# Kernel tuning notes

Hardware: AMD Instinct MI355X
Metric: run time of the kernel (lower is better)

The kernel has to match this reference:

```python
import jax, jax.numpy as jnp
import numpy as np

B, S, D_MODEL = 2, 2048, 2048
H, DS, DG, DV = 16, 64, 64, 128
ROPE_BASE = 10000.0
NEG_INF = -1e9


def _rope(x, base=ROPE_BASE):
    # x: [B, S, H, D] -> rotate-half RoPE over positions 0..S-1
    d = x.shape[-1]
    half = d // 2
    inv_freq = 1.0 / (base ** (jnp.arange(half, dtype=jnp.float32) / half))
    ang = jnp.arange(x.shape[1], dtype=jnp.float32)[:, None] * inv_freq  # [S, half]
    cos = jnp.cos(ang)[None, :, None, :]
    sin = jnp.sin(ang)[None, :, None, :]
    x1, x2 = x[..., :half], x[..., half:]
    return jnp.concatenate([x1 * cos - x2 * sin, x1 * sin + x2 * cos], axis=-1)


def setup_inputs() -> dict:
    key = jax.random.key(0)
    ks = jax.random.split(key, 8)
    s = lambda fan_in: 1.0 / np.sqrt(fan_in)
    return {
        "x": jax.random.normal(ks[0], (B, S, D_MODEL), dtype=jnp.float32),
        "wq_sem": jax.random.normal(ks[1], (D_MODEL, H * DS), dtype=jnp.float32) * s(D_MODEL),
        "wk_sem": jax.random.normal(ks[2], (D_MODEL, H * DS), dtype=jnp.float32) * s(D_MODEL),
        "wq_geo": jax.random.normal(ks[3], (D_MODEL, H * DG), dtype=jnp.float32) * s(D_MODEL),
        "wk_geo": jax.random.normal(ks[4], (D_MODEL, H * DG), dtype=jnp.float32) * s(D_MODEL),
        "wv": jax.random.normal(ks[5], (D_MODEL, H * DV), dtype=jnp.float32) * s(D_MODEL),
        "wo": jax.random.normal(ks[6], (H * DV, D_MODEL), dtype=jnp.float32) * s(H * DV),
        "gate_logit": jax.random.normal(ks[7], (H,), dtype=jnp.float32),
    }


def reference(x, wq_sem, wk_sem, wq_geo, wk_geo, wv, wo, gate_logit):
    b, sl, _ = x.shape
    # Projections -> [B, S, H, d]
    qs = (x @ wq_sem).reshape(b, sl, H, DS)
    ksem = (x @ wk_sem).reshape(b, sl, H, DS)
    qg = _rope((x @ wq_geo).reshape(b, sl, H, DG))
    kg = _rope((x @ wk_geo).reshape(b, sl, H, DG))
    v = (x @ wv).reshape(b, sl, H, DV)

    sem_scale = 1.0 / np.sqrt(DS)
    geo_scale = 1.0 / np.sqrt(DG)
    sem_scores = jnp.einsum("bqhd,bkhd->bhqk", qs, ksem) * sem_scale
    geo_scores = jnp.einsum("bqhd,bkhd->bhqk", qg, kg) * geo_scale

    # Learned per-head gate mixing semantic vs geometric paths
    g = jax.nn.sigmoid(gate_logit)[None, :, None, None]
    scores = g * sem_scores + (1.0 - g) * geo_scores

    causal = jnp.tril(jnp.ones((sl, sl), dtype=bool))
    scores = jnp.where(causal[None, None], scores, NEG_INF)
    attn = jax.nn.softmax(scores, axis=-1)

    out = jnp.einsum("bhqk,bkhd->bqhd", attn, v).reshape(b, sl, H * DV)
    return out @ wo
```

## Files before the change

kernel.cpp:

```cpp
#include <hip/hip_runtime.h>
#include <hip/hip_bf16.h>

typedef unsigned short u16;
typedef __attribute__((ext_vector_type(4))) float floatx4;
typedef __attribute__((ext_vector_type(8))) __bf16 bf16x8;

__device__ __forceinline__ u16 f2bf(float f) {
  unsigned int x = __builtin_bit_cast(unsigned int, f);
  unsigned int r = (x + 0x7fffu + ((x >> 16) & 1u)) >> 16;
  return (u16)r;
}
__device__ __forceinline__ float bf2f(u16 u) {
  unsigned int x = ((unsigned int)u) << 16;
  return __builtin_bit_cast(float, x);
}
__device__ __forceinline__ floatx4 mfma16(bf16x8 a, bf16x8 b, floatx4 c) {
  return __builtin_amdgcn_mfma_f32_16x16x32_bf16(a, b, c, 0, 0, 0);
}
__device__ __forceinline__ void gload16(const u16* g, u16* l) {
  __builtin_amdgcn_global_load_lds(
      (const __attribute__((address_space(1))) unsigned int*)g,
      (__attribute__((address_space(3))) unsigned int*)l, 16, 0, 0);
}
#define SCHEDB() __builtin_amdgcn_sched_barrier(0)
#define SBAR() __builtin_amdgcn_s_barrier()

#define BB 2
#define SS 2048
#define DM 2048
#define HH 16
#define PCOLS 6144

__global__ void prep_all_k(const float* __restrict__ x,
                           const float* w0, const float* w1, const float* w2,
                           const float* w3, const float* w4, const float* w5,
                           u16* __restrict__ WcatT, u16* __restrict__ WoT,
                           u16* __restrict__ Xbf,
                           float* __restrict__ cosT, float* __restrict__ sinT) {
  const int z = blockIdx.z;
  const int tx = threadIdx.x, ty = threadIdx.y;
  const int ftid = ty * 32 + tx;

  if (z == 6) {
    size_t base = ((size_t)(blockIdx.y * 64 + blockIdx.x)) * 2048 + (size_t)ftid * 8;
    float4 v0 = *(const float4*)&x[base];
    float4 v1 = *(const float4*)&x[base + 4];
    ushort4 o0, o1;
    o0.x = f2bf(v0.x); o0.y = f2bf(v0.y); o0.z = f2bf(v0.z); o0.w = f2bf(v0.w);
    o1.x = f2bf(v1.x); o1.y = f2bf(v1.y); o1.z = f2bf(v1.z); o1.w = f2bf(v1.w);
    *(ushort4*)&Xbf[base] = o0;
    *(ushort4*)&Xbf[base + 4] = o1;
    return;
  }
  if (z == 7) {
    int lb = blockIdx.y * 64 + blockIdx.x;
    if (lb >= 256) return;
    int idx = lb * 256 + ftid;
    int s = idx >> 5, d = idx & 31;
    double inv = pow(10000.0, -(double)d / 32.0);
    double ang = (double)s * inv;
    cosT[idx] = (float)cos(ang);
    sinT[idx] = (float)sin(ang);
    return;
  }

  __shared__ float tile[32][33];
  const float* src; u16* dst; int cols;
  if (z == 0)      { src = w0; dst = WcatT;                        cols = 1024; }
  else if (z == 1) { src = w1; dst = WcatT + (size_t)1024 * 2048;  cols = 1024; }
  else if (z == 2) { src = w2; dst = WcatT + (size_t)2048 * 2048;  cols = 1024; }
  else if (z == 3) { src = w3; dst = WcatT + (size_t)3072 * 2048;  cols = 1024; }
  else if (z == 4) { src = w4; dst = WcatT + (size_t)4096 * 2048;  cols = 2048; }
  else             { src = w5; dst = WoT;                          cols = 2048; }
  int c0 = blockIdx.x * 32;
  if (c0 >= cols) return;
  int r0 = blockIdx.y * 32;
#pragma unroll
  for (int i = 0; i < 4; ++i)
    tile[ty + i * 8][tx] = src[(size_t)(r0 + ty + i * 8) * cols + c0 + tx];
  __syncthreads();
#pragma unroll
  for (int i = 0; i < 4; ++i)
    dst[(size_t)(c0 + ty + i * 8) * 2048 + r0 + tx] = f2bf(tile[tx][ty + i * 8]);
}

__global__ void ropevt_k(u16* __restrict__ P, const float* __restrict__ cosT,
                         const float* __restrict__ sinT, u16* __restrict__ VtG) {
  const int bid = blockIdx.x;
  const int tid = threadIdx.x;
  if (bid < 16384) {
    int idx = bid * 256 + tid;
    int d = idx & 31, h = (idx >> 5) & 15, reg = (idx >> 9) & 1, row = idx >> 10;
    int s = row & (SS - 1);
    size_t base = (size_t)row * PCOLS + (reg ? 3072 : 2048) + h * 64 + d;
    float x1 = bf2f(P[base]), x2 = bf2f(P[base + 32]);
    float c = cosT[s * 32 + d], sn = sinT[s * 32 + d];
    P[base] = f2bf(x1 * c - x2 * sn);
    P[base + 32] = f2bf(x1 * sn + x2 * c);
    return;
  }
  __shared__ u16 t[32][33];
  int b2 = bid - 16384;
  int b = b2 >> 12;
  int s0 = ((b2 >> 6) & 63) * 32;
  int c0 = (b2 & 63) * 32;
  int tx = tid & 31, ty = tid >> 5;
#pragma unroll
  for (int i = 0; i < 4; ++i)
    t[ty + i * 8][tx] = P[((size_t)b * SS + s0 + ty + i * 8) * PCOLS + 4096 + c0 + tx];
  __syncthreads();
#pragma unroll
  for (int i = 0; i < 4; ++i)
    VtG[((size_t)b * 2048 + c0 + ty + i * 8) * SS + s0 + tx] = t[tx][ty + i * 8];
}

template <int NFB, bool OUTF32>
__global__ __launch_bounds__(256, 1)
void gemm4_k(const u16* __restrict__ A, const u16* __restrict__ Bt,
             void* __restrict__ Cout, int M, int N, int K) {
  constexpr int BH = NFB / 2;
  __shared__ alignas(16) u16 lds[16384 + NFB * 8192];
  const int tid = threadIdx.x;
  const int wid = tid >> 6, lane = tid & 63;
  const int lr = lane & 15, lg = lane >> 4;
  const int m0 = blockIdx.y * 128, n0 = blockIdx.x * (NFB * 64);
  const int NT = K >> 6;
  const int NSLAB = NT * 4;

  const int aoff = lr * 32 + ((lg ^ ((lr >> 1) & 3)) * 8);

  const int srow = wid * 16 + (lane >> 2);
  const int sgl = (((lane & 3) ^ ((lane >> 3) & 3)) * 8);
  const u16* Asrc = A + (size_t)(m0 + srow) * K + sgl;
  const u16* Bsrc = Bt + (size_t)(n0 + srow) * K + sgl;

  floatx4 acc[8][NFB];
#pragma unroll
  for (int m = 0; m < 8; ++m)
#pragma unroll
    for (int n = 0; n < NFB; ++n) acc[m][n] = (floatx4){0.f, 0.f, 0.f, 0.f};

  auto stgA = [&](int tile, int kh) {
    u16* d = lds + ((tile & 1) * 2 + kh) * 4096 + wid * 512;
    const u16* s = Asrc + tile * 64 + kh * 32;
#pragma unroll
    for (int c = 0; c < 2; ++c) gload16(s + (size_t)(c * 64) * K, d + c * 2048);
  };
  auto stgB = [&](int tile, int kh) {
    u16* d = lds + 16384 + ((tile & 1) * 2 + kh) * (NFB * 2048) + wid * 512;
    const u16* s = Bsrc + tile * 64 + kh * 32;
#pragma unroll
    for (int c = 0; c < NFB; ++c) gload16(s + (size_t)(c * 64) * K, d + c * 2048);
  };
  auto stage_slab = [&](int s) {
    if (s >= NSLAB) return;
    int tile = s >> 2, kind = s & 3;
    if (kind == 0) stgA(tile, 0);
    else if (kind == 1) stgB(tile, 0);
    else if (kind == 2) stgA(tile, 1);
    else stgB(tile, 1);
  };

  for (int s = 0; s < 7; ++s) stage_slab(s);
  if constexpr (NFB == 6) asm volatile("s_waitcnt vmcnt(10)" ::: "memory");
  else                    asm volatile("s_waitcnt vmcnt(8)" ::: "memory");
  SCHEDB(); SBAR(); SCHEDB();

  bf16x8 af[8], bfv[BH];

#pragma unroll 1
  for (int it = 0; it < (NT >> 1); ++it) {
    const int t = it * 2;
    const int sb = t * 4 + 6;
    const bool more = (t + 2 < NT);

#define PH(BUF, KK, NH, SL, DOVM)                                               \
    {                                                                           \
      const u16* Ab = lds + ((BUF) * 2 + (KK)) * 4096;                          \
      const u16* Bb = lds + 16384 + ((BUF) * 2 + (KK)) * (NFB * 2048);          \
      if ((NH) == 0) {                                                          \
        _Pragma("unroll") for (int m = 0; m < 8; ++m)                           \
          af[m] = *(const bf16x8*)&Ab[(m * 16) * 32 + aoff];                    \
      }                                                                         \
      _Pragma("unroll") for (int j = 0; j < BH; ++j)                            \
        bfv[j] = *(const bf16x8*)&Bb[(wid * NFB * 16 + ((NH) * BH + j) * 16) * 32 + aoff]; \
      stage_slab(sb + (SL));                                                    \
      SCHEDB(); SBAR(); SCHEDB();                                               \
      __builtin_amdgcn_s_setprio(1);                                            \
      _Pragma("unroll") for (int m = 0; m < 8; ++m)                             \
        _Pragma("unroll") for (int j = 0; j < BH; ++j)                          \
          acc[m][(NH) * BH + j] = mfma16(af[m], bfv[j], acc[m][(NH) * BH + j]); \
      __builtin_amdgcn_s_setprio(0);                                            \
      if (DOVM) {                                                               \
        if (more) {                                                             \
          if constexpr (NFB == 6) asm volatile("s_waitcnt vmcnt(10)" ::: "memory"); \
          else                    asm volatile("s_waitcnt vmcnt(8)" ::: "memory");  \
        } else {                                                                \
          asm volatile("s_waitcnt vmcnt(0)" ::: "memory");                      \
        }                                                                       \
      }                                                                         \
      SCHEDB(); SBAR(); SCHEDB();                                               \
    }

    PH(0, 0, 0, 1, 0)
    PH(0, 0, 1, 2, 0)
    PH(0, 1, 0, 3, 0)
    PH(0, 1, 1, 4, 1)
    PH(1, 0, 0, 5, 0)
    PH(1, 0, 1, 6, 0)
    PH(1, 1, 0, 7, 0)
    PH(1, 1, 1, 8, 1)
#undef PH
  }

#pragma unroll
  for (int m = 0; m < 8; ++m) {
    int row0 = m0 + m * 16 + lg * 4;
#pragma unroll
    for (int n = 0; n < NFB; ++n) {
      int col = n0 + wid * NFB * 16 + n * 16 + lr;
#pragma unroll
      for (int r = 0; r < 4; ++r) {
        size_t off = (size_t)(row0 + r) * N + col;
        if (OUTF32) ((float*)Cout)[off] = acc[m][n][r];
        else        ((u16*)Cout)[off] = f2bf(acc[m][n][r]);
      }
    }
  }
}

__device__ __forceinline__ bf16x8 load_scaled(const u16* p, float s) {
  uint4 raw = *(const uint4*)p;
  const u16* ru = (const u16*)&raw;
  bf16x8 out;
#pragma unroll
  for (int j = 0; j < 8; ++j) out[j] = (__bf16)(bf2f(ru[j]) * s);
  return out;
}

__global__ __launch_bounds__(256, 3)
void attn_k(const u16* __restrict__ P, const u16* __restrict__ VtG,
            const float* __restrict__ gate, u16* __restrict__ AttO) {
  const int pairi = blockIdx.x >> 4;
  const int h = blockIdx.x & 15;
  const int b = blockIdx.y;
  const int tid = threadIdx.x, wid = tid >> 6, lane = tid & 63;
  const int lr = lane & 15, lg = lane >> 4;
  const size_t rowb = (size_t)b * SS;

  const float g = 1.f / (1.f + __expf(-gate[h]));
  const float ssc = g * 0.125f;
  const float gsc = (1.f - g) * 0.125f;

  __shared__ alignas(16) u16 Ks[64 * 64];
  __shared__ alignas(16) u16 Kg[64 * 64];
  __shared__ alignas(16) u16 Vt[128 * 64];
  __shared__ alignas(16) u16 Pw[4][16 * 64];

  const int strow = tid >> 3;
  const int stg = ((tid & 7) ^ (strow & 7)) * 8;
  const int swz = lr & 7;

  for (int half = 0; half < 2; ++half) {
    const int qb = half ? (31 - pairi) : pairi;
    const int q0 = qb * 64;

    const u16* qbase = P + (rowb + q0 + wid * 16 + lr) * PCOLS + h * 64;
    bf16x8 qs[2], qg[2];
#pragma unroll
    for (int kk = 0; kk < 2; ++kk) {
      qs[kk] = load_scaled(qbase + kk * 32 + lg * 8, ssc);
      qg[kk] = load_scaled(qbase + 2048 + kk * 32 + lg * 8, gsc);
    }

    float m_r = -1e30f, l_r = 0.f;
    floatx4 o[8];
#pragma unroll
    for (int n = 0; n < 8; ++n) o[n] = (floatx4){0.f, 0.f, 0.f, 0.f};

    const int nkv = q0 + 64;
    for (int kv0 = 0; kv0 < nkv; kv0 += 64) {
      __syncthreads();
      {
        const u16* ks = P + (rowb + kv0 + strow) * PCOLS + 1024 + h * 64 + stg;
        const u16* gs = P + (rowb + kv0 + strow) * PCOLS + 3072 + h * 64 + stg;
        gload16(ks, Ks + wid * 512);
        gload16(gs, Kg + wid * 512);
        gload16(ks + (size_t)32 * PCOLS, Ks + 2048 + wid * 512);
        gload16(gs + (size_t)32 * PCOLS, Kg + 2048 + wid * 512);
      }
      {
        const u16* vs = VtG + ((size_t)b * 2048 + h * 128 + strow) * SS + kv0 + stg;
#pragma unroll
        for (int c = 0; c < 4; ++c)
          gload16(vs + (size_t)(c * 32) * SS, Vt + c * 2048 + wid * 512);
      }
      __syncthreads();

      floatx4 sc[4];
#pragma unroll
      for (int s = 0; s < 4; ++s) sc[s] = (floatx4){0.f, 0.f, 0.f, 0.f};
#pragma unroll
      for (int kk = 0; kk < 2; ++kk) {
#pragma unroll
        for (int s = 0; s < 4; ++s) {
          bf16x8 kf = *(const bf16x8*)&Ks[(s * 16 + lr) * 64 + ((kk * 4 + lg) ^ swz) * 8];
          bf16x8 gf = *(const bf16x8*)&Kg[(s * 16 + lr) * 64 + ((kk * 4 + lg) ^ swz) * 8];
          sc[s] = mfma16(kf, qs[kk], sc[s]);
          sc[s] = mfma16(gf, qg[kk], sc[s]);
        }
      }

      const int qrow = q0 + wid * 16 + lr;
      const bool needmask = (kv0 + 63 > q0 + wid * 16);
      float vv[4][4];
      float vmax = -1e30f;
#pragma unroll
      for (int s = 0; s < 4; ++s)
#pragma unroll
        for (int r = 0; r < 4; ++r) {
          float val = sc[s][r];
          if (needmask) val = (kv0 + s * 16 + lg * 4 + r <= qrow) ? val : -1e30f;
          vv[s][r] = val;
          vmax = fmaxf(vmax, val);
        }
      vmax = fmaxf(vmax, __shfl_xor(vmax, 16));
      vmax = fmaxf(vmax, __shfl_xor(vmax, 32));

      const bool defer = __all(vmax - m_r <= 8.0f);
      const float mnew = defer ? m_r : fmaxf(m_r, vmax);
      float psum = 0.f;
#pragma unroll
      for (int s = 0; s < 4; ++s)
#pragma unroll
        for (int r = 0; r < 4; ++r) {
          vv[s][r] = __expf(vv[s][r] - mnew);
          psum += vv[s][r];
        }
      psum += __shfl_xor(psum, 16);
      psum += __shfl_xor(psum, 32);

#pragma unroll
      for (int s = 0; s < 4; ++s)
#pragma unroll
        for (int t = 0; t < 2; ++t) {
          unsigned int w;
          asm("v_cvt_pk_bf16_f32 %0, %1, %2" : "=v"(w) : "v"(vv[s][2 * t]), "v"(vv[s][2 * t + 1]));
          int u16off = lr * 64 + ((s * 2 + (lg >> 1)) ^ swz) * 8 + (lg & 1) * 4 + t * 2;
          *(unsigned int*)&Pw[wid][u16off] = w;
        }

      if (!defer) {
        float corr = __expf(m_r - mnew);
        l_r *= corr;
        m_r = mnew;
        float crr[4];
#pragma unroll
        for (int r = 0; r < 4; ++r) crr[r] = __shfl(corr, lg * 4 + r);
#pragma unroll
        for (int n = 0; n < 8; ++n)
#pragma unroll
          for (int r = 0; r < 4; ++r) o[n][r] *= crr[r];
      }
      l_r += psum;

      asm volatile("s_waitcnt lgkmcnt(0)" ::: "memory");
      SCHEDB();
      bf16x8 pa0 = *(const bf16x8*)&Pw[wid][lr * 64 + (lg ^ swz) * 8];
      bf16x8 pa1 = *(const bf16x8*)&Pw[wid][lr * 64 + ((4 + lg) ^ swz) * 8];
#pragma unroll
      for (int n = 0; n < 8; ++n) {
        bf16x8 vb0 = *(const bf16x8*)&Vt[(n * 16 + lr) * 64 + (lg ^ swz) * 8];
        bf16x8 vb1 = *(const bf16x8*)&Vt[(n * 16 + lr) * 64 + ((4 + lg) ^ swz) * 8];
        o[n] = mfma16(pa0, vb0, o[n]);
        o[n] = mfma16(pa1, vb1, o[n]);
      }
    }

    float linv = 1.f / l_r;
    float lnv[4];
#pragma unroll
    for (int r = 0; r < 4; ++r) lnv[r] = __shfl(linv, lg * 4 + r);
#pragma unroll
    for (int n = 0; n < 8; ++n)
#pragma unroll
      for (int r = 0; r < 4; ++r) {
        float val = o[n][r] * lnv[r];
        AttO[(rowb + q0 + wid * 16 + lg * 4 + r) * (size_t)(HH * 128) + h * 128 + n * 16 + lr] =
            f2bf(val);
      }
  }
}

extern "C" void kernel_launch(void* const* d_in, const int* in_sizes, int n_in,
                              void* d_out, int out_size, void* d_ws, size_t ws_size,
                              hipStream_t stream) {
  const float* x       = (const float*)d_in[0];
  const float* wq_sem  = (const float*)d_in[1];
  const float* wk_sem  = (const float*)d_in[2];
  const float* wq_geo  = (const float*)d_in[3];
  const float* wk_geo  = (const float*)d_in[4];
  const float* wv      = (const float*)d_in[5];
  const float* wo      = (const float*)d_in[6];
  const float* gate    = (const float*)d_in[7];

  char* ws = (char*)d_ws;
  u16* Xbf   = (u16*)(ws);
  u16* WcatT = (u16*)(ws + 16777216);
  u16* WoT   = (u16*)(ws + 16777216 + 25165824);
  u16* P     = (u16*)(ws + 16777216 + 25165824 + 8388608);
  float* cosT = (float*)(ws + 16777216 + 25165824 + 8388608 + 50331648);
  float* sinT = cosT + 2048 * 32;
  u16* AttO = Xbf;
  u16* VtG  = WcatT;

  dim3 tb(32, 8);
  prep_all_k<<<dim3(64, 64, 8), tb, 0, stream>>>(x, wq_sem, wk_sem, wq_geo, wk_geo,
                                                 wv, wo, WcatT, WoT, Xbf, cosT, sinT);

  gemm4_k<6, false><<<dim3(16, 32), 256, 0, stream>>>(Xbf, WcatT, P, 4096, 6144, 2048);
  ropevt_k<<<24576, 256, 0, stream>>>(P, cosT, sinT, VtG);
  attn_k<<<dim3(256, 2), 256, 0, stream>>>(P, VtG, gate, AttO);
  gemm4_k<4, true><<<dim3(8, 32), 256, 0, stream>>>(AttO, WoT, d_out, 4096, 2048, 2048);
}
```

Measured before the change: 258.7 us.

## Fuse V transpose into projection GEMM epilogue and vectorize RoPE kernel

The projection GEMM epilogue now writes the V columns straight into a transposed VtG buffer with 4-element vector stores. This removes the separate LDS transpose pass and shrinks P to 4096 columns. The RoPE kernel is rewritten to process 8 elements per thread with 128-bit loads and stores, using far fewer blocks. The attention kernel also raises wave priority around its MFMA loops so matrix work is issued ahead of other waves. The transposed epilogue stores are strided across rows, which may coalesce less well than the old transpose kernel.

```diff
diff --git a/kernel.cpp b/kernel.cpp
--- a/kernel.cpp
+++ b/kernel.cpp
@@ -29,7 +29,7 @@
 #define SS 2048
 #define DM 2048
 #define HH 16
-#define PCOLS 6144
+#define PCOLS 4096
 
 __global__ void prep_all_k(const float* __restrict__ x,
                            const float* w0, const float* w1, const float* w2,
@@ -84,40 +84,37 @@
     dst[(size_t)(c0 + ty + i * 8) * 2048 + r0 + tx] = f2bf(tile[tx][ty + i * 8]);
 }
 
-__global__ void ropevt_k(u16* __restrict__ P, const float* __restrict__ cosT,
-                         const float* __restrict__ sinT, u16* __restrict__ VtG) {
-  const int bid = blockIdx.x;
-  const int tid = threadIdx.x;
-  if (bid < 16384) {
-    int idx = bid * 256 + tid;
-    int d = idx & 31, h = (idx >> 5) & 15, reg = (idx >> 9) & 1, row = idx >> 10;
-    int s = row & (SS - 1);
-    size_t base = (size_t)row * PCOLS + (reg ? 3072 : 2048) + h * 64 + d;
-    float x1 = bf2f(P[base]), x2 = bf2f(P[base + 32]);
-    float c = cosT[s * 32 + d], sn = sinT[s * 32 + d];
-    P[base] = f2bf(x1 * c - x2 * sn);
-    P[base + 32] = f2bf(x1 * sn + x2 * c);
-    return;
-  }
-  __shared__ u16 t[32][33];
-  int b2 = bid - 16384;
-  int b = b2 >> 12;
-  int s0 = ((b2 >> 6) & 63) * 32;
-  int c0 = (b2 & 63) * 32;
-  int tx = tid & 31, ty = tid >> 5;
-#pragma unroll
-  for (int i = 0; i < 4; ++i)
-    t[ty + i * 8][tx] = P[((size_t)b * SS + s0 + ty + i * 8) * PCOLS + 4096 + c0 + tx];
-  __syncthreads();
-#pragma unroll
-  for (int i = 0; i < 4; ++i)
-    VtG[((size_t)b * 2048 + c0 + ty + i * 8) * SS + s0 + tx] = t[tx][ty + i * 8];
-}
-
-template <int NFB, bool OUTF32>
+__global__ void rope_k(u16* __restrict__ P, const float* __restrict__ cosT,
+                       const float* __restrict__ sinT) {
+  int idx = blockIdx.x * 256 + threadIdx.x;
+  int d0 = (idx & 3) * 8;
+  int h = (idx >> 2) & 15, reg = (idx >> 6) & 1, row = idx >> 7;
+  int s = row & (SS - 1);
+  size_t base = (size_t)row * PCOLS + (reg ? 3072 : 2048) + h * 64 + d0;
+  uint4 x1 = *(const uint4*)&P[base];
+  uint4 x2 = *(const uint4*)&P[base + 32];
+  const u16* x1v = (const u16*)&x1;
+  const u16* x2v = (const u16*)&x2;
+  float cv[8], sv[8];
+  *(float4*)&cv[0] = *(const float4*)&cosT[s * 32 + d0];
+  *(float4*)&cv[4] = *(const float4*)&cosT[s * 32 + d0 + 4];
+  *(float4*)&sv[0] = *(const float4*)&sinT[s * 32 + d0];
+  *(float4*)&sv[4] = *(const float4*)&sinT[s * 32 + d0 + 4];
+  u16 o1v[8], o2v[8];
+#pragma unroll
+  for (int j = 0; j < 8; ++j) {
+    float a1 = bf2f(x1v[j]), a2 = bf2f(x2v[j]);
+    o1v[j] = f2bf(a1 * cv[j] - a2 * sv[j]);
+    o2v[j] = f2bf(a1 * sv[j] + a2 * cv[j]);
+  }
+  *(uint4*)&P[base] = *(const uint4*)o1v;
+  *(uint4*)&P[base + 32] = *(const uint4*)o2v;
+}
+
+template <int NFB, bool OUTF32, bool VSPLIT>
 __global__ __launch_bounds__(256, 1)
 void gemm4_k(const u16* __restrict__ A, const u16* __restrict__ Bt,
-             void* __restrict__ Cout, int M, int N, int K) {
+             void* __restrict__ Cout, u16* __restrict__ VtGo, int M, int N, int K) {
   constexpr int BH = NFB / 2;
   __shared__ alignas(16) u16 lds[16384 + NFB * 8192];
   const int tid = threadIdx.x;
@@ -219,11 +216,25 @@
 #pragma unroll
     for (int n = 0; n < NFB; ++n) {
       int col = n0 + wid * NFB * 16 + n * 16 + lr;
-#pragma unroll
-      for (int r = 0; r < 4; ++r) {
-        size_t off = (size_t)(row0 + r) * N + col;
-        if (OUTF32) ((float*)Cout)[off] = acc[m][n][r];
-        else        ((u16*)Cout)[off] = f2bf(acc[m][n][r]);
+      if constexpr (VSPLIT) {
+        if (col < 4096) {
+#pragma unroll
+          for (int r = 0; r < 4; ++r)
+            ((u16*)Cout)[(size_t)(row0 + r) * 4096 + col] = f2bf(acc[m][n][r]);
+        } else {
+          ushort4 o;
+          o.x = f2bf(acc[m][n][0]); o.y = f2bf(acc[m][n][1]);
+          o.z = f2bf(acc[m][n][2]); o.w = f2bf(acc[m][n][3]);
+          int bb = row0 >> 11, s = row0 & (SS - 1);
+          *(ushort4*)&VtGo[((size_t)bb * 2048 + (col - 4096)) * SS + s] = o;
+        }
+      } else {
+#pragma unroll
+        for (int r = 0; r < 4; ++r) {
+          size_t off = (size_t)(row0 + r) * N + col;
+          if (OUTF32) ((float*)Cout)[off] = acc[m][n][r];
+          else        ((u16*)Cout)[off] = f2bf(acc[m][n][r]);
+        }
       }
     }
   }
@@ -300,6 +311,7 @@
       floatx4 sc[4];
 #pragma unroll
       for (int s = 0; s < 4; ++s) sc[s] = (floatx4){0.f, 0.f, 0.f, 0.f};
+      __builtin_amdgcn_s_setprio(1);
 #pragma unroll
       for (int kk = 0; kk < 2; ++kk) {
 #pragma unroll
@@ -310,6 +322,7 @@
           sc[s] = mfma16(gf, qg[kk], sc[s]);
         }
       }
+      __builtin_amdgcn_s_setprio(0);
 
       const int qrow = q0 + wid * 16 + lr;
       const bool needmask = (kv0 + 63 > q0 + wid * 16);
@@ -368,6 +381,7 @@
       SCHEDB();
       bf16x8 pa0 = *(const bf16x8*)&Pw[wid][lr * 64 + (lg ^ swz) * 8];
       bf16x8 pa1 = *(const bf16x8*)&Pw[wid][lr * 64 + ((4 + lg) ^ swz) * 8];
+      __builtin_amdgcn_s_setprio(1);
 #pragma unroll
       for (int n = 0; n < 8; ++n) {
         bf16x8 vb0 = *(const bf16x8*)&Vt[(n * 16 + lr) * 64 + (lg ^ swz) * 8];
@@ -375,6 +389,7 @@
         o[n] = mfma16(pa0, vb0, o[n]);
         o[n] = mfma16(pa1, vb1, o[n]);
       }
+      __builtin_amdgcn_s_setprio(0);
     }
 
     float linv = 1.f / l_r;
@@ -407,19 +422,21 @@
   char* ws = (char*)d_ws;
   u16* Xbf   = (u16*)(ws);
   u16* WcatT = (u16*)(ws + 16777216);
-  u16* WoT   = (u16*)(ws + 16777216 + 25165824);
-  u16* P     = (u16*)(ws + 16777216 + 25165824 + 8388608);
-  float* cosT = (float*)(ws + 16777216 + 25165824 + 8388608 + 50331648);
+  u16* WoT   = (u16*)(ws + 41943040);
+  u16* P     = (u16*)(ws + 50331648);
+  u16* VtG   = (u16*)(ws + 83886080);
+  float* cosT = (float*)(ws + 100663296);
   float* sinT = cosT + 2048 * 32;
   u16* AttO = Xbf;
-  u16* VtG  = WcatT;
 
   dim3 tb(32, 8);
   prep_all_k<<<dim3(64, 64, 8), tb, 0, stream>>>(x, wq_sem, wk_sem, wq_geo, wk_geo,
                                                  wv, wo, WcatT, WoT, Xbf, cosT, sinT);
 
-  gemm4_k<6, false><<<dim3(16, 32), 256, 0, stream>>>(Xbf, WcatT, P, 4096, 6144, 2048);
-  ropevt_k<<<24576, 256, 0, stream>>>(P, cosT, sinT, VtG);
+  gemm4_k<6, false, true><<<dim3(16, 32), 256, 0, stream>>>(Xbf, WcatT, P, VtG,
+                                                            4096, 6144, 2048);
+  rope_k<<<2048, 256, 0, stream>>>(P, cosT, sinT);
   attn_k<<<dim3(256, 2), 256, 0, stream>>>(P, VtG, gate, AttO);
-  gemm4_k<4, true><<<dim3(8, 32), 256, 0, stream>>>(AttO, WoT, d_out, 4096, 2048, 2048);
-}
+  gemm4_k<4, true, false><<<dim3(8, 32), 256, 0, stream>>>(AttO, WoT, d_out, nullptr,
+                                                           4096, 2048, 2048);
+}
```

Result: faster. 250.5 us (-3.1%).
